# Kernel optimization log

Measured on AMD Instinct MI355X. Metric: run time of the kernel, lower is better.

The kernel has to match this reference:

```python
import jax, jax.numpy as jnp
import numpy as np

B, N, C_IN, C_OUT = 2, 163842, 64, 64  # icosphere level-7 vertex count
K = 7  # 1-ring neighborhood size (center + 6 neighbors)


def setup_inputs() -> dict:
    key = jax.random.key(0)
    kx, kw, kb, kn = jax.random.split(key, 4)
    x = jax.random.normal(kx, (B, N, C_IN), dtype=jnp.float32)
    # nn.Linear(7*in_feats, out_feats): W is (out, 7*in), bias (out,)
    W = jax.random.normal(kw, (C_OUT, K * C_IN), dtype=jnp.float32) * (1.0 / np.sqrt(K * C_IN))
    b = jax.random.normal(kb, (C_OUT,), dtype=jnp.float32) * 0.01
    neigh_orders = jax.random.randint(kn, (K * N,), 0, N, dtype=jnp.int64)
    return {"x": x, "W": W, "b": b, "neigh_orders": neigh_orders}


def reference(x, W, b, neigh_orders):
    # Faithful translation of onering_conv_layer_batch.forward:
    #   x: (B, N, C) -> permute -> (B, C, N)
    #   gather 7N indices on vertex axis -> (B, C, 7N)
    #   view -> (B, N, 7C)  (raw reshape of the (C, 7N) block, as in the torch code)
    #   Linear(7C -> out)
    Bb, Nn, Cc = x.shape
    xp = jnp.transpose(x, (0, 2, 1))            # (B, C, N)
    g = jnp.take(xp, neigh_orders, axis=2)      # (B, C, 7N)
    mat = g.reshape(Bb, Nn, K * Cc)             # (B, N, 7C)
    return jnp.einsum('bnk,ok->bno', mat, W) + b
```

## Files before the change

kernel.cpp:

```cpp
#include <hip/hip_runtime.h>

typedef short bf8_t __attribute__((ext_vector_type(8)));
typedef float f32x4 __attribute__((ext_vector_type(4)));

static constexpr int Bc      = 2;
static constexpr int Nv      = 163842;
static constexpr int CIN     = 64;
static constexpr int COUT    = 64;
static constexpr int KK      = 448;
static constexpr int SEVEN_N = 7 * Nv;
static constexpr int THREADS = 512;

static constexpr int LM      = 3 * KK;
static constexpr int MST     = LM + KK;
static constexpr int STRIDE  = 1800;
static constexpr int NT      = (SEVEN_N + LM - 1) / LM;
static constexpr int NPAIR   = MST / 2;
static constexpr int TILE_SH = 16 * STRIDE + 32;

__device__ inline int cbase(int c) {
    return c * STRIDE + 32 * (c >> 3);
}

__device__ inline unsigned pack2_bf16(float a, float b) {
    unsigned ua = __builtin_bit_cast(unsigned, a);
    unsigned ub = __builtin_bit_cast(unsigned, b);
    ua = (ua + 0x7FFFu + ((ua >> 16) & 1u)) >> 16;
    ub = (ub + 0x7FFFu + ((ub >> 16) & 1u));
    return (ua & 0xFFFFu) | (ub & 0xFFFF0000u);
}

__global__ __launch_bounds__(256) void xconv(const float* __restrict__ x,
                                             short* __restrict__ xb, int n) {
    const int i = (blockIdx.x * 256 + threadIdx.x) * 8;
    if (i >= n) return;
    const float4 a = *(const float4*)(x + i);
    const float4 c = *(const float4*)(x + i + 4);
    uint4 o;
    o.x = pack2_bf16(a.x, a.y); o.y = pack2_bf16(a.z, a.w);
    o.z = pack2_bf16(c.x, c.y); o.w = pack2_bf16(c.z, c.w);
    *(uint4*)(xb + i) = o;
}

__global__ __launch_bounds__(THREADS, 4) void conv_main_bf16(
    const short* __restrict__ xbf,
    const short* __restrict__ Wb,
    const float* __restrict__ bias,
    const int*   __restrict__ idx,
    float*       __restrict__ out)
{
    __shared__ short tile[TILE_SH];

    const int bid   = blockIdx.x;
    const int s     = bid & 7;
    const int b     = s & 1;
    const int mtres = s >> 1;
    const int rr    = bid >> 3;
    const int mt    = (rr >> 2) * 4 + mtres;
    const int cg    = rr & 3;
    if (mt >= NT) return;

    const int t    = threadIdx.x;
    const int M0   = mt * LM;
    const int mEnd = min(M0 + MST, SEVEN_N);
    const short* xb = xbf + (size_t)b * Nv * CIN;

    const int q     = t & 1;
    const int pidl  = t >> 1;
    const int choff = cg * 16 + q * 8;

    int2 ivp[4];
    #pragma unroll
    for (int p = 0; p < 4; ++p) {
        const int pp = p * 256 + pidl;
        const int m0 = M0 + 2 * pp;
        if (pp < NPAIR && m0 + 1 < SEVEN_N) {
            ivp[p] = *(const int2*)(idx + m0);
        } else if (pp < NPAIR && m0 < SEVEN_N) {
            ivp[p].x = idx[m0]; ivp[p].y = idx[m0];
        } else {
            ivp[p].x = 0; ivp[p].y = 0;
        }
    }
    bf8_t v0[4], v1[4];
    #pragma unroll
    for (int p = 0; p < 4; ++p) {
        v0[p] = *(const bf8_t*)(xb + (size_t)ivp[p].x * CIN + choff);
        v1[p] = *(const bf8_t*)(xb + (size_t)ivp[p].y * CIN + choff);
    }

    const int lane = t & 63;
    const int w    = t >> 6;
    const int col  = lane & 15;
    const int hi   = lane >> 4;
    const int oc   = w & 3;
    const short* wbase = Wb + (oc * 16 + col) * KK + 8 * hi;
    bf8_t bfrag[14];
    #pragma unroll
    for (int k0 = 0; k0 < 14; ++k0)
        bfrag[k0] = *(const bf8_t*)(wbase + 32 * k0);

    #pragma unroll
    for (int p = 0; p < 4; ++p) {
        const int pp = p * 256 + pidl;
        const int m0 = M0 + 2 * pp;
        if (pp < NPAIR && m0 < mEnd) {
            const int dm = 2 * pp;
            #pragma unroll
            for (int j = 0; j < 8; ++j) {
                const int c     = q * 8 + j;
                const int shift = (6 * c) & 7;
                const unsigned lo = (unsigned short)v0[p][j];
                const unsigned hi2 = (unsigned short)v1[p][j];
                *(unsigned*)&tile[cbase(c) + dm + shift] = lo | (hi2 << 16);
            }
        }
    }
    __syncthreads();

    const int Ca  = cg * 16 + col;
    const int Ta  = Ca * SEVEN_N + M0;
    const int d0a = (448 - (Ta % 448)) % 448;
    const int sha = Ta & 7;
    const short* abase0 = &tile[cbase(col) + d0a + sha + 8 * hi];
    const float bo = bias[oc * 16 + col];

    for (int task = w; task < 12; task += 8) {
        const int r = task >> 2;
        const short* abase = abase0 + 448 * r;

        f32x4 acc = (f32x4){0.f, 0.f, 0.f, 0.f};
        #pragma unroll
        for (int k0 = 0; k0 < 14; ++k0) {
            const bf8_t afrag = *(const bf8_t*)(abase + 32 * k0);
            acc = __builtin_amdgcn_mfma_f32_16x16x32_bf16(afrag, bfrag[k0], acc, 0, 0, 0);
        }
        #pragma unroll
        for (int i = 0; i < 4; ++i) {
            const int c_s = 4 * hi + i;
            const int Cs  = cg * 16 + c_s;
            const int Ts  = Cs * SEVEN_N + M0;
            const int d0s = (448 - (Ts % 448)) % 448;
            const int sr  = M0 + d0s + 448 * r;
            if (sr + 448 <= SEVEN_N) {
                const int n = (Ts + d0s) / 448 + r;
                out[((size_t)b * Nv + n) * COUT + oc * 16 + col] = acc[i] + bo;
            }
        }
    }
}

static constexpr int PAIRS   = MST / 2;
static constexpr int PPP     = THREADS / 4;
static constexpr int PASSES  = PAIRS / PPP;

__global__ __launch_bounds__(THREADS, 4) void conv_main_f32(
    const float* __restrict__ x,
    const short* __restrict__ Wb,
    const float* __restrict__ bias,
    const int*   __restrict__ idx,
    float*       __restrict__ out)
{
    __shared__ short tile[16 * STRIDE];

    const int bid  = blockIdx.x;
    const int slot = bid & 7;
    const int cg   = slot >> 1;
    const int b    = slot & 1;
    const int mt   = bid >> 3;
    const int t    = threadIdx.x;
    const int M0   = mt * LM;
    const int mEnd = min(M0 + MST, SEVEN_N);
    const float* xb = x + (size_t)b * Nv * CIN;

    const int q    = t & 3;
    const int pidl = t >> 2;
    const int xoff = cg * 16 + q * 4;

    int iv0[PASSES], iv1[PASSES];
    #pragma unroll
    for (int p = 0; p < PASSES; ++p) {
        const int m0 = M0 + 2 * (p * PPP + pidl);
        const bool ok = (m0 < mEnd);
        iv0[p] = ok ? idx[m0] : 0;
        iv1[p] = (ok && m0 + 1 < mEnd) ? idx[m0 + 1] : 0;
    }
    float4 v0[PASSES], v1[PASSES];
    #pragma unroll
    for (int p = 0; p < PASSES; ++p) {
        v0[p] = *(const float4*)(xb + (size_t)iv0[p] * CIN + xoff);
        v1[p] = *(const float4*)(xb + (size_t)iv1[p] * CIN + xoff);
    }
    #pragma unroll
    for (int p = 0; p < PASSES; ++p) {
        const int m0 = M0 + 2 * (p * PPP + pidl);
        if (m0 < mEnd) {
            const float a0[4] = {v0[p].x, v0[p].y, v0[p].z, v0[p].w};
            const float a1[4] = {v1[p].x, v1[p].y, v1[p].z, v1[p].w};
            #pragma unroll
            for (int i = 0; i < 4; ++i) {
                const int c     = q * 4 + i;
                const int shift = (6 * c) & 7;
                const int ppos  = (m0 - M0) + shift;
                *(unsigned*)&tile[c * STRIDE + ppos] = pack2_bf16(a0[i], a1[i]);
            }
        }
    }
    __syncthreads();

    const int lane = t & 63;
    const int w    = t >> 6;
    const int col  = lane & 15;
    const int hi   = lane >> 4;
    const int oc   = w & 3;

    const short* wbase = Wb + (oc * 16 + col) * KK + 8 * hi;
    bf8_t bfrag[14];
    #pragma unroll
    for (int k0 = 0; k0 < 14; ++k0)
        bfrag[k0] = *(const bf8_t*)(wbase + 32 * k0);

    const int Ca  = cg * 16 + col;
    const int Ta  = Ca * SEVEN_N + M0;
    const int d0a = (448 - (Ta % 448)) % 448;
    const int sha = Ta & 7;
    const short* abase0 = &tile[col * STRIDE + d0a + sha + 8 * hi];
    const float bo = bias[oc * 16 + col];

    for (int task = w; task < 12; task += 8) {
        const int r = task >> 2;
        const short* abase = abase0 + 448 * r;
        f32x4 acc = (f32x4){0.f, 0.f, 0.f, 0.f};
        #pragma unroll
        for (int k0 = 0; k0 < 14; ++k0) {
            const bf8_t afrag = *(const bf8_t*)(abase + 32 * k0);
            acc = __builtin_amdgcn_mfma_f32_16x16x32_bf16(afrag, bfrag[k0], acc, 0, 0, 0);
        }
        #pragma unroll
        for (int i = 0; i < 4; ++i) {
            const int c_s = 4 * hi + i;
            const int Cs  = cg * 16 + c_s;
            const int Ts  = Cs * SEVEN_N + M0;
            const int d0s = (448 - (Ts % 448)) % 448;
            const int sr  = M0 + d0s + 448 * r;
            if (sr + 448 <= SEVEN_N) {
                const int n = (Ts + d0s) / 448 + r;
                out[((size_t)b * Nv + n) * COUT + oc * 16 + col] = acc[i] + bo;
            }
        }
    }
}

__global__ __launch_bounds__(256) void conv_cleanup(
    const float* __restrict__ x,
    const float* __restrict__ W,
    const float* __restrict__ bias,
    const int*   __restrict__ idx,
    float*       __restrict__ out)
{
    __shared__ float part[4][64];
    const int C = blockIdx.x;
    const int b = blockIdx.y;
    const int t = threadIdx.x;
    const int o = t & 63;
    const int p = t >> 6;
    const int n = (int)(((long long)(C + 1) * SEVEN_N + 447) / 448) - 1;
    const int s = 448 * n - C * SEVEN_N;
    if (s + 448 <= SEVEN_N) return;
    const float* xb = x + (size_t)b * Nv * CIN;
    float acc = 0.f;
    for (int j = p * 112; j < (p + 1) * 112; ++j) {
        int m = s + j, c = C;
        if (m >= SEVEN_N) { m -= SEVEN_N; c += 1; }
        acc += xb[(size_t)idx[m] * CIN + c] * W[o * KK + j];
    }
    part[p][o] = acc;
    __syncthreads();
    if (p == 0)
        out[((size_t)b * Nv + n) * COUT + o] =
            part[0][o] + part[1][o] + part[2][o] + part[3][o] + bias[o];
}

__global__ void wconv(const float* __restrict__ W, short* __restrict__ Wb) {
    const int i = blockIdx.x * 256 + threadIdx.x;
    if (i < COUT * KK) {
        unsigned u = __builtin_bit_cast(unsigned, W[i]);
        u = (u + 0x7FFFu + ((u >> 16) & 1u)) >> 16;
        Wb[i] = (short)u;
    }
}

extern "C" void kernel_launch(void* const* d_in, const int* in_sizes, int n_in,
                              void* d_out, int out_size, void* d_ws, size_t ws_size,
                              hipStream_t stream) {
    const float* x    = (const float*)d_in[0];
    const float* W    = (const float*)d_in[1];
    const float* bias = (const float*)d_in[2];
    const int*   idx  = (const int*)d_in[3];
    float*       out  = (float*)d_out;
    short*       Wb   = (short*)d_ws;

    hipLaunchKernelGGL(wconv, dim3((COUT * KK + 255) / 256), dim3(256), 0, stream, W, Wb);

    const int    nxe  = Bc * Nv * CIN;
    const size_t need = 65536 + (size_t)nxe * sizeof(short);
    if (ws_size >= need) {
        short* xbf = (short*)((char*)d_ws + 65536);
        hipLaunchKernelGGL(xconv, dim3((nxe / 8 + 255) / 256), dim3(256), 0, stream,
                           x, xbf, nxe);
        hipLaunchKernelGGL(conv_main_bf16, dim3(214 * 4 * 8), dim3(THREADS), 0, stream,
                           xbf, Wb, bias, idx, out);
    } else {
        hipLaunchKernelGGL(conv_main_f32, dim3(NT * 8), dim3(THREADS), 0, stream,
                           x, Wb, bias, idx, out);
    }
    hipLaunchKernelGGL(conv_cleanup, dim3(CIN, Bc), dim3(256), 0, stream,
                       x, W, bias, idx, out);
}
```

Measured before the change: 186.9 us.

## Pre-shift bf16 tile per channel to shrink LDS and raise occupancy

After: 371.8 us. 99.0% more time.

```diff
diff --git a/kernel.cpp b/kernel.cpp
--- a/kernel.cpp
+++ b/kernel.cpp
@@ -13,14 +13,10 @@
 
 static constexpr int LM      = 3 * KK;
 static constexpr int MST     = LM + KK;
-static constexpr int STRIDE  = 1800;
 static constexpr int NT      = (SEVEN_N + LM - 1) / LM;
 static constexpr int NPAIR   = MST / 2;
-static constexpr int TILE_SH = 16 * STRIDE + 32;
-
-__device__ inline int cbase(int c) {
-    return c * STRIDE + 32 * (c >> 3);
-}
+static constexpr int CST     = 1352;
+static constexpr int TILE_SH = 16 * CST;
 
 __device__ inline unsigned pack2_bf16(float a, float b) {
     unsigned ua = __builtin_bit_cast(unsigned, a);
@@ -42,7 +38,7 @@
     *(uint4*)(xb + i) = o;
 }
 
-__global__ __launch_bounds__(THREADS, 4) void conv_main_bf16(
+__global__ __launch_bounds__(THREADS, 6) void conv_main_bf16(
     const short* __restrict__ xbf,
     const short* __restrict__ Wb,
     const float* __restrict__ bias,
@@ -69,18 +65,28 @@
     const int pidl  = t >> 1;
     const int choff = cg * 16 + q * 8;
 
+    int d0a_[8];
+    int lo = 1 << 30, hiR = 0;
+    {
+        int r448 = (int)(((unsigned)choff * (unsigned)SEVEN_N + (unsigned)M0) % 448u);
+        #pragma unroll
+        for (int j = 0; j < 8; ++j) {
+            d0a_[j] = r448 ? 448 - r448 : 0;
+            lo  = min(lo, d0a_[j]);
+            hiR = max(hiR, d0a_[j]);
+            r448 += 14; if (r448 >= 448) r448 -= 448;
+        }
+    }
+
     int2 ivp[4];
+    bool okp[4];
     #pragma unroll
     for (int p = 0; p < 4; ++p) {
         const int pp = p * 256 + pidl;
-        const int m0 = M0 + 2 * pp;
-        if (pp < NPAIR && m0 + 1 < SEVEN_N) {
-            ivp[p] = *(const int2*)(idx + m0);
-        } else if (pp < NPAIR && m0 < SEVEN_N) {
-            ivp[p].x = idx[m0]; ivp[p].y = idx[m0];
-        } else {
-            ivp[p].x = 0; ivp[p].y = 0;
-        }
+        const int dm = 2 * pp;
+        const int m0 = M0 + dm;
+        okp[p] = (pp < NPAIR) && (m0 < mEnd) && (dm + 1 >= lo) && (dm <= hiR + 1343);
+        ivp[p] = okp[p] ? *(const int2*)(idx + m0) : make_int2(0, 0);
     }
     bf8_t v0[4], v1[4];
     #pragma unroll
@@ -102,27 +108,23 @@
 
     #pragma unroll
     for (int p = 0; p < 4; ++p) {
-        const int pp = p * 256 + pidl;
-        const int m0 = M0 + 2 * pp;
-        if (pp < NPAIR && m0 < mEnd) {
-            const int dm = 2 * pp;
+        if (okp[p]) {
+            const int dm = 2 * (p * 256 + pidl);
             #pragma unroll
             for (int j = 0; j < 8; ++j) {
-                const int c     = q * 8 + j;
-                const int shift = (6 * c) & 7;
-                const unsigned lo = (unsigned short)v0[p][j];
-                const unsigned hi2 = (unsigned short)v1[p][j];
-                *(unsigned*)&tile[cbase(c) + dm + shift] = lo | (hi2 << 16);
+                const int c  = q * 8 + j;
+                const int pj = dm - d0a_[j];
+                if ((unsigned)pj < (unsigned)LM) {
+                    const unsigned lov = (unsigned short)v0[p][j];
+                    const unsigned hiv = (unsigned short)v1[p][j];
+                    *(unsigned*)&tile[c * CST + pj] = lov | (hiv << 16);
+                }
             }
         }
     }
     __syncthreads();
 
-    const int Ca  = cg * 16 + col;
-    const int Ta  = Ca * SEVEN_N + M0;
-    const int d0a = (448 - (Ta % 448)) % 448;
-    const int sha = Ta & 7;
-    const short* abase0 = &tile[cbase(col) + d0a + sha + 8 * hi];
+    const short* abase0 = &tile[col * CST + 8 * hi];
     const float bo = bias[oc * 16 + col];
 
     for (int task = w; task < 12; task += 8) {
@@ -150,9 +152,9 @@
     }
 }
 
-static constexpr int PAIRS   = MST / 2;
+static constexpr int STRIDE3 = 1800;
 static constexpr int PPP     = THREADS / 4;
-static constexpr int PASSES  = PAIRS / PPP;
+static constexpr int PASSES  = NPAIR / PPP;
 
 __global__ __launch_bounds__(THREADS, 4) void conv_main_f32(
     const float* __restrict__ x,
@@ -161,7 +163,7 @@
     const int*   __restrict__ idx,
     float*       __restrict__ out)
 {
-    __shared__ short tile[16 * STRIDE];
+    __shared__ short tile[16 * STRIDE3];
 
     const int bid  = blockIdx.x;
     const int slot = bid & 7;
@@ -202,7 +204,7 @@
                 const int c     = q * 4 + i;
                 const int shift = (6 * c) & 7;
                 const int ppos  = (m0 - M0) + shift;
-                *(unsigned*)&tile[c * STRIDE + ppos] = pack2_bf16(a0[i], a1[i]);
+                *(unsigned*)&tile[c * STRIDE3 + ppos] = pack2_bf16(a0[i], a1[i]);
             }
         }
     }
@@ -224,7 +226,7 @@
     const int Ta  = Ca * SEVEN_N + M0;
     const int d0a = (448 - (Ta % 448)) % 448;
     const int sha = Ta & 7;
-    const short* abase0 = &tile[col * STRIDE + d0a + sha + 8 * hi];
+    const short* abase0 = &tile[col * STRIDE3 + d0a + sha + 8 * hi];
     const float bo = bias[oc * 16 + col];
 
     for (int task = w; task < 12; task += 8) {
```
